# Kernel tuning notes

Measured on AMD Instinct MI355X. Metric: run time of the kernel, lower is better.

The kernel has to match this reference:

```python
import jax, jax.numpy as jnp
import numpy as np

B, S, D = 2, 4096, 1152
H = 16
HD = D // H  # 72
SCALE = HD ** -0.5


def setup_inputs() -> dict:
    key = jax.random.key(0)
    ks = jax.random.split(key, 9)
    std = 1.0 / np.sqrt(D)
    return {
        "x": jax.random.normal(ks[0], (B, S, D), dtype=jnp.float32),
        "q_w": jax.random.normal(ks[1], (D, D), dtype=jnp.float32) * std,
        "q_b": jax.random.normal(ks[2], (D,), dtype=jnp.float32) * std,
        "k_w": jax.random.normal(ks[3], (D, D), dtype=jnp.float32) * std,
        "k_b": jax.random.normal(ks[4], (D,), dtype=jnp.float32) * std,
        "v_w": jax.random.normal(ks[5], (D, D), dtype=jnp.float32) * std,
        "v_b": jax.random.normal(ks[6], (D,), dtype=jnp.float32) * std,
        "o_w": jax.random.normal(ks[7], (D, D), dtype=jnp.float32) * std,
        "o_b": jax.random.normal(ks[8], (D,), dtype=jnp.float32) * std,
    }


def reference(x, q_w, q_b, k_w, k_b, v_w, v_b, o_w, o_b):
    # Linear layers: torch nn.Linear stores weight as [out, in]; y = x @ W^T + b
    q = jnp.einsum("bsd,ed->bse", x, q_w) + q_b
    k = jnp.einsum("bsd,ed->bse", x, k_w) + k_b
    v = jnp.einsum("bsd,ed->bse", x, v_w) + v_b
    # [B, H, S, HD]
    q = q.reshape(B, S, H, HD).transpose(0, 2, 1, 3)
    k = k.reshape(B, S, H, HD).transpose(0, 2, 1, 3)
    v = v.reshape(B, S, H, HD).transpose(0, 2, 1, 3)
    # scores [B, H, S, S]
    scores = jnp.einsum("bhqd,bhkd->bhqk", q, k) * SCALE
    attn = jax.nn.softmax(scores.astype(jnp.float32), axis=-1).astype(q.dtype)
    out = jnp.einsum("bhqk,bhkd->bhqd", attn, v)
    out = out.transpose(0, 2, 1, 3).reshape(B, S, D)
    return jnp.einsum("bsd,ed->bse", out, o_w) + o_b
```

## Files before the change

### kernel.cpp

```cpp
#include <hip/hip_runtime.h>

#define NB 2
#define NS 4096
#define ND 1152
#define NH 16
#define HD 72
#define HP 80
#define VP 96
#define QSCALE (0.11785113019775793f * 1.4426950408889634f)

typedef float f32x4 __attribute__((ext_vector_type(4)));
typedef float f32x16 __attribute__((ext_vector_type(16)));
typedef __bf16 bf16x8 __attribute__((ext_vector_type(8)));
typedef unsigned short u16x8 __attribute__((ext_vector_type(8)));
typedef unsigned short u16x4 __attribute__((ext_vector_type(4)));
typedef unsigned int u32x4 __attribute__((ext_vector_type(4)));

__device__ __forceinline__ unsigned short f2bf(float f) {
  return __builtin_bit_cast(unsigned short, (__bf16)f);
}
__device__ __forceinline__ bf16x8 asbf(u16x8 u) {
  return __builtin_bit_cast(bf16x8, u);
}
__device__ __forceinline__ unsigned cvtpk(float lo, float hi) {
  unsigned d;
  asm("v_cvt_pk_bf16_f32 %0, %1, %2" : "=v"(d) : "v"(lo), "v"(hi));
  return d;
}
__device__ __forceinline__ void lane32swap(unsigned &x, unsigned &y) {
  asm volatile("v_permlane32_swap_b32 %0, %1" : "+v"(x), "+v"(y));
}
#if __has_builtin(__builtin_amdgcn_exp2f)
#define EXP2(x) __builtin_amdgcn_exp2f(x)
#else
#define EXP2(x) exp2f(x)
#endif
__device__ __forceinline__ void gll16(const void* g, void* l) {
  __builtin_amdgcn_global_load_lds(
      (__attribute__((address_space(1))) void*)(unsigned long long)g,
      (__attribute__((address_space(3))) void*)l, 16, 0, 0);
}

__global__ __launch_bounds__(256) void cvt_all(
    const float* __restrict__ x,
    const float* __restrict__ qw, const float* __restrict__ kw,
    const float* __restrict__ vw,
    unsigned short* __restrict__ xb, unsigned short* __restrict__ wb) {
  const size_t NX = (size_t)8192 * ND;
  const size_t NW = (size_t)ND * ND;
  size_t i = ((size_t)blockIdx.x * 256 + threadIdx.x) * 8;
  const float* s; unsigned short* d; size_t off;
  if (i < NX)            { s = x;  d = xb;          off = i; }
  else if (i < NX + NW)  { s = qw; d = wb;          off = i - NX; }
  else if (i < NX + 2*NW){ s = kw; d = wb + NW;     off = i - NX - NW; }
  else                   { s = vw; d = wb + 2 * NW; off = i - NX - 2 * NW; }
  f32x4 a = *(const f32x4*)(s + off);
  f32x4 b = *(const f32x4*)(s + off + 4);
  u16x8 o;
#pragma unroll
  for (int j = 0; j < 4; ++j) { o[j] = f2bf(a[j]); o[j + 4] = f2bf(b[j]); }
  *(u16x8*)(d + off) = o;
}

__global__ __launch_bounds__(256) void pad_zero(unsigned short* __restrict__ q80,
                                                unsigned short* __restrict__ k80,
                                                unsigned short* __restrict__ vt) {
  int i = blockIdx.x * 256 + threadIdx.x;
  u16x8 z = {};
  if (i < 131072) {
    *(u16x8*)(q80 + (size_t)i * HP + HD) = z;
  } else if (i < 262144) {
    *(u16x8*)(k80 + (size_t)(i - 131072) * HP + HD) = z;
  } else {
    int j = i - 262144;
    int bh = j / 12288;
    int r = j % 12288;
    int row = 72 + r / 512;
    int col = (r % 512) * 8;
    u16x8 v = z;
    if (row == HD) {
#pragma unroll
      for (int j8 = 0; j8 < 8; ++j8) v[j8] = 0x3F80;
    }
    *(u16x8*)(vt + ((size_t)bh * VP + row) * NS + col) = v;
  }
}

__global__ __launch_bounds__(256) void qk_gemm(
    const unsigned short* __restrict__ xb, const unsigned short* __restrict__ wb,
    const float* __restrict__ qbias, const float* __restrict__ kbias,
    unsigned short* __restrict__ qp, unsigned short* __restrict__ kp)
{
  const int mb = blockIdx.x * 128;
  const int nb = blockIdx.y * 128;
  const int proj = blockIdx.z;
  const unsigned short* w = wb + (size_t)proj * (ND * ND);
  const float* bias = proj == 0 ? qbias : kbias;

  __shared__ __align__(16) unsigned short la[128 * 64];
  __shared__ __align__(16) unsigned short lb[128 * 64];

  const int t = threadIdx.x;
  const int lane = t & 63;
  const int wid = t >> 6;
  const int mo = (wid >> 1) * 64, no = (wid & 1) * 64;
  const int l15 = lane & 15, l4 = lane >> 4;

  const unsigned short* ga = xb + (size_t)(mb + wid * 32 + (lane >> 3)) * ND + (lane & 7) * 8;
  const unsigned short* gb = w  + (size_t)(nb + wid * 32 + (lane >> 3)) * ND + (lane & 7) * 8;

  f32x4 acc[4][4] = {};

  for (int kt = 0; kt < ND / 64; ++kt) {
    const int k0 = kt * 64;
    __syncthreads();
#pragma unroll
    for (int j = 0; j < 4; ++j) {
      gll16(ga + (size_t)j * 8 * ND + k0, &la[(wid * 4 + j) * 512]);
      gll16(gb + (size_t)j * 8 * ND + k0, &lb[(wid * 4 + j) * 512]);
    }
    __syncthreads();
#pragma unroll
    for (int ks = 0; ks < 2; ++ks) {
      bf16x8 af[4], bfr[4];
#pragma unroll
      for (int mt = 0; mt < 4; ++mt)
        af[mt] = asbf(*(const u16x8*)(&la[(mo + mt * 16 + l15) * 64 + ks * 32 + l4 * 8]));
#pragma unroll
      for (int nt = 0; nt < 4; ++nt)
        bfr[nt] = asbf(*(const u16x8*)(&lb[(no + nt * 16 + l15) * 64 + ks * 32 + l4 * 8]));
#pragma unroll
      for (int mt = 0; mt < 4; ++mt)
#pragma unroll
        for (int nt = 0; nt < 4; ++nt)
          acc[mt][nt] = __builtin_amdgcn_mfma_f32_16x16x32_bf16(af[mt], bfr[nt], acc[mt][nt], 0, 0, 0);
    }
  }

#pragma unroll
  for (int mt = 0; mt < 4; ++mt) {
#pragma unroll
    for (int nt = 0; nt < 4; ++nt) {
      const int n = nb + no + nt * 16 + l15;
      const float bval = bias[n];
      const int h = n / HD, hd = n % HD;
#pragma unroll
      for (int r = 0; r < 4; ++r) {
        const int m = mb + mo + mt * 16 + l4 * 4 + r;
        const int b = m >> 12, sl = m & (NS - 1);
        const int bh = b * NH + h;
        float v = acc[mt][nt][r] + bval;
        if (proj == 0)
          qp[((size_t)bh * NS + sl) * HP + hd] = f2bf(v * QSCALE);
        else
          kp[((size_t)bh * NS + sl) * HP + hd] = f2bf(v);
      }
    }
  }
}

__global__ __launch_bounds__(256) void v_gemm(
    const unsigned short* __restrict__ xb, const unsigned short* __restrict__ wv,
    const float* __restrict__ vb, unsigned short* __restrict__ vt)
{
  const int mb = blockIdx.x * 128;
  const int nb = blockIdx.y * 128;

  __shared__ __align__(16) unsigned short la[128 * 64];
  __shared__ __align__(16) unsigned short lb[128 * 64];

  const int t = threadIdx.x;
  const int lane = t & 63;
  const int wid = t >> 6;
  const int mo = (wid >> 1) * 64, no = (wid & 1) * 64;
  const int l15 = lane & 15, l4 = lane >> 4;

  const unsigned short* ga = xb + (size_t)(mb + wid * 32 + (lane >> 3)) * ND + (lane & 7) * 8;
  const unsigned short* gb = wv + (size_t)(nb + wid * 32 + (lane >> 3)) * ND + (lane & 7) * 8;

  f32x4 acc[4][4] = {};

  for (int kt = 0; kt < ND / 64; ++kt) {
    const int k0 = kt * 64;
    __syncthreads();
#pragma unroll
    for (int j = 0; j < 4; ++j) {
      gll16(ga + (size_t)j * 8 * ND + k0, &la[(wid * 4 + j) * 512]);
      gll16(gb + (size_t)j * 8 * ND + k0, &lb[(wid * 4 + j) * 512]);
    }
    __syncthreads();
#pragma unroll
    for (int ks = 0; ks < 2; ++ks) {
      bf16x8 af[4], bfr[4];
#pragma unroll
      for (int mt = 0; mt < 4; ++mt)
        af[mt] = asbf(*(const u16x8*)(&la[(mo + mt * 16 + l15) * 64 + ks * 32 + l4 * 8]));
#pragma unroll
      for (int nt = 0; nt < 4; ++nt)
        bfr[nt] = asbf(*(const u16x8*)(&lb[(no + nt * 16 + l15) * 64 + ks * 32 + l4 * 8]));
#pragma unroll
      for (int mt = 0; mt < 4; ++mt)
#pragma unroll
        for (int nt = 0; nt < 4; ++nt)
          acc[mt][nt] = __builtin_amdgcn_mfma_f32_16x16x32_bf16(bfr[nt], af[mt], acc[mt][nt], 0, 0, 0);
    }
  }

#pragma unroll
  for (int mt = 0; mt < 4; ++mt) {
    const int m = mb + mo + mt * 16 + l15;
    const int b = m >> 12, sl = m & (NS - 1);
#pragma unroll
    for (int nt = 0; nt < 4; ++nt) {
#pragma unroll
      for (int r = 0; r < 4; ++r) {
        const int n = nb + no + nt * 16 + l4 * 4 + r;
        const int h = n / HD, hd = n % HD;
        vt[(((size_t)(b * NH + h)) * VP + hd) * NS + sl] =
            f2bf(acc[mt][nt][r] + vb[n]);
      }
    }
  }
}

__device__ __forceinline__ void softmax_pv(f32x16 s, const unsigned short* cur,
                                           int mt, int lane, f32x16 o[3]) {
#pragma unroll
  for (int i = 0; i < 16; ++i) s[i] = EXP2(s[i]);
  unsigned dk[8];
#pragma unroll
  for (int r2 = 0; r2 < 4; ++r2) {
    dk[2 * r2]     = cvtpk(s[4 * r2],     s[4 * r2 + 1]);
    dk[2 * r2 + 1] = cvtpk(s[4 * r2 + 2], s[4 * r2 + 3]);
  }
#pragma unroll
  for (int a = 0; a < 2; ++a) {
    unsigned x0 = dk[4 * a + 0], y0 = dk[4 * a + 2];
    unsigned x1 = dk[4 * a + 1], y1 = dk[4 * a + 3];
    lane32swap(x0, y0);
    lane32swap(x1, y1);
    u32x4 wd = {x0, x1, y0, y1};
    bf16x8 pf = __builtin_bit_cast(bf16x8, wd);
    const int ks2 = mt * 2 + a;
    __builtin_amdgcn_s_setprio(1);
#pragma unroll
    for (int hdt = 0; hdt < 3; ++hdt) {
      bf16x8 vf = asbf(*(const u16x8*)(&cur[(640 + (hdt * 4 + ks2) * 64 + lane) * 8]));
      o[hdt] = __builtin_amdgcn_mfma_f32_32x32x16_bf16(vf, pf, o[hdt], 0, 0, 0);
    }
    __builtin_amdgcn_s_setprio(0);
  }
}

__global__ __launch_bounds__(512, 4) void attn_fwd(
    const unsigned short* __restrict__ qp,
    const unsigned short* __restrict__ kp,
    const unsigned short* __restrict__ vt,
    unsigned short* __restrict__ ao)
{
  const int d = blockIdx.x;
  const int qt = (d >> 3) & 15;
  const int bh = (d & 7) + 8 * (d >> 7);
  const int b = bh >> 4, h = bh & 15;
  const int qs0 = qt * 256;

  __shared__ __align__(16) unsigned short sm[2 * 1408 * 8];

  const int t = threadIdx.x;
  const int wv = t >> 6;
  const int lane = t & 63;
  const int q = lane & 31;
  const int hh = lane >> 5;

  bf16x8 qf[5];
  {
    const unsigned short* qrow =
        qp + ((size_t)bh * NS + qs0 + wv * 32 + q) * HP + hh * 8;
#pragma unroll
    for (int ks = 0; ks < 5; ++ks)
      qf[ks] = asbf(*(const u16x8*)(qrow + ks * 16));
  }

  const unsigned short* kb0 = kp + (size_t)bh * NS * HP;
  const unsigned short* vb0 = vt + (size_t)bh * VP * NS;
  const unsigned short* gp[3];
  int stp[3], goff[3];
  const bool has2 = wv < 6;
#pragma unroll
  for (int j = 0; j < 3; ++j) {
    int g = wv + 8 * j;
    if (g > 21) g = 21;
    if (g < 10) {
      gp[j] = kb0 + ((g / 5) * 32 + (lane & 31)) * HP + (g % 5) * 16 + (lane >> 5) * 8;
      stp[j] = 64 * HP;
    } else {
      const int f = g - 10;
      gp[j] = vb0 + (size_t)((f >> 2) * 32 + (lane & 31)) * NS + (f & 3) * 16 + (lane >> 5) * 8;
      stp[j] = 64;
    }
    goff[j] = g * 512;
  }

  f32x16 o[3] = {};

  gll16(gp[0], sm + goff[0]); gp[0] += stp[0];
  gll16(gp[1], sm + goff[1]); gp[1] += stp[1];
  if (has2) { gll16(gp[2], sm + goff[2]); gp[2] += stp[2]; }
  __syncthreads();

  for (int it = 0; it < NS / 64; ++it) {
    unsigned short* cur = sm + (it & 1) * 11264;
    unsigned short* nxt = sm + ((it + 1) & 1) * 11264;
    if (it < NS / 64 - 1) {
      gll16(gp[0], nxt + goff[0]); gp[0] += stp[0];
      gll16(gp[1], nxt + goff[1]); gp[1] += stp[1];
      if (has2) { gll16(gp[2], nxt + goff[2]); gp[2] += stp[2]; }
    }

#pragma unroll
    for (int mt = 0; mt < 2; ++mt) {
      f32x16 s = {};
      __builtin_amdgcn_s_setprio(1);
#pragma unroll
      for (int ks = 0; ks < 5; ++ks) {
        bf16x8 kf = asbf(*(const u16x8*)(&cur[((mt * 5 + ks) * 64 + lane) * 8]));
        s = __builtin_amdgcn_mfma_f32_32x32x16_bf16(kf, qf[ks], s, 0, 0, 0);
      }
      __builtin_amdgcn_s_setprio(0);
      softmax_pv(s, cur, mt, lane, o);
    }
    __syncthreads();
  }

  const float l_tot = __shfl(o[2][4], q);
  const float inv = 1.0f / l_tot;
  const int srow = qs0 + wv * 32 + q;
  unsigned short* ob = ao + ((size_t)b * NS + srow) * ND + h * HD;
#pragma unroll
  for (int hdt = 0; hdt < 3; ++hdt)
#pragma unroll
    for (int r2 = 0; r2 < 4; ++r2) {
      const int hd0 = hdt * 32 + r2 * 8 + hh * 4;
      if (hd0 < HD) {
        u16x4 ov;
#pragma unroll
        for (int r0 = 0; r0 < 4; ++r0) ov[r0] = f2bf(o[hdt][r2 * 4 + r0] * inv);
        *(u16x4*)(ob + hd0) = ov;
      }
    }
}

__global__ __launch_bounds__(256) void oproj_gemm(
    const unsigned short* __restrict__ a,
    const float* __restrict__ w, const float* __restrict__ bias,
    float* __restrict__ out)
{
  const int mb = blockIdx.x * 128;
  const int nb = blockIdx.y * 128;

  __shared__ __align__(16) unsigned short la[128 * 72];
  __shared__ __align__(16) unsigned short lb[128 * 72];

  const int t = threadIdx.x;
  const int lane = t & 63;
  const int wid = t >> 6;
  const int mo = (wid >> 1) * 64, no = (wid & 1) * 64;
  const int l15 = lane & 15, l4 = lane >> 4;

  f32x4 acc[4][4] = {};

  for (int kt = 0; kt < ND / 64; ++kt) {
    const int k0 = kt * 64;
    __syncthreads();
#pragma unroll
    for (int i = 0; i < 4; ++i) {
      int c = t + i * 256;
      int row = c >> 3, c8 = c & 7;
      u16x8 ua = *(const u16x8*)(a + (size_t)(mb + row) * ND + k0 + c8 * 8);
      *(u16x8*)(&la[row * 72 + c8 * 8]) = ua;
    }
#pragma unroll
    for (int i = 0; i < 8; ++i) {
      int c = t + i * 256;
      int row = c >> 4, c4 = c & 15;
      f32x4 b4 = *(const f32x4*)(w + (size_t)(nb + row) * ND + k0 + c4 * 4);
      u16x4 ub;
#pragma unroll
      for (int j = 0; j < 4; ++j) ub[j] = f2bf(b4[j]);
      *(u16x4*)(&lb[row * 72 + c4 * 4]) = ub;
    }
    __syncthreads();
#pragma unroll
    for (int ks = 0; ks < 2; ++ks) {
      bf16x8 af[4], bfr[4];
#pragma unroll
      for (int mt = 0; mt < 4; ++mt)
        af[mt] = asbf(*(const u16x8*)(&la[(mo + mt * 16 + l15) * 72 + ks * 32 + l4 * 8]));
#pragma unroll
      for (int nt = 0; nt < 4; ++nt)
        bfr[nt] = asbf(*(const u16x8*)(&lb[(no + nt * 16 + l15) * 72 + ks * 32 + l4 * 8]));
#pragma unroll
      for (int mt = 0; mt < 4; ++mt)
#pragma unroll
        for (int nt = 0; nt < 4; ++nt)
          acc[mt][nt] = __builtin_amdgcn_mfma_f32_16x16x32_bf16(af[mt], bfr[nt], acc[mt][nt], 0, 0, 0);
    }
  }

#pragma unroll
  for (int mt = 0; mt < 4; ++mt)
#pragma unroll
    for (int nt = 0; nt < 4; ++nt) {
      const int n = nb + no + nt * 16 + l15;
      const float bval = bias[n];
#pragma unroll
      for (int r = 0; r < 4; ++r) {
        const int m = mb + mo + mt * 16 + l4 * 4 + r;
        out[(size_t)m * ND + n] = acc[mt][nt][r] + bval;
      }
    }
}

extern "C" void kernel_launch(void* const* d_in, const int* in_sizes, int n_in,
                              void* d_out, int out_size, void* d_ws, size_t ws_size,
                              hipStream_t stream) {
  const float* x  = (const float*)d_in[0];
  const float* qw = (const float*)d_in[1];
  const float* qb = (const float*)d_in[2];
  const float* kw = (const float*)d_in[3];
  const float* kb = (const float*)d_in[4];
  const float* vw = (const float*)d_in[5];
  const float* vb = (const float*)d_in[6];
  const float* ow = (const float*)d_in[7];
  const float* ob = (const float*)d_in[8];
  float* out = (float*)d_out;

  char* ws = (char*)d_ws;
  unsigned short* q80    = (unsigned short*)(ws);
  unsigned short* k80    = (unsigned short*)(ws + 20971520);
  unsigned short* v_t    = (unsigned short*)(ws + 41943040);
  unsigned short* xb     = (unsigned short*)(ws + 67108864);
  unsigned short* wb     = (unsigned short*)(ws + 85983232);

  cvt_all<<<dim3(6552), dim3(256), 0, stream>>>(x, qw, kw, vw, xb, wb);
  pad_zero<<<dim3(2560), dim3(256), 0, stream>>>(q80, k80, v_t);
  qk_gemm<<<dim3(64, 9, 2), dim3(256), 0, stream>>>(xb, wb, qb, kb, q80, k80);
  v_gemm<<<dim3(64, 9), dim3(256), 0, stream>>>(xb, wb + 2 * (size_t)ND * ND,
                                                vb, v_t);
  attn_fwd<<<dim3(512), dim3(512), 0, stream>>>(q80, k80, v_t, xb );
  oproj_gemm<<<dim3(64, 9), dim3(256), 0, stream>>>(xb , ow, ob, out);
}
```

Before: 350.4 us.

## Merge cvt/pad kernels, convert o_w in attention tail blocks, use LDS DMA in oproj

Fuses the conversion and padding kernels into one launch to save a launch. Adds 16 extra blocks to the attention grid that convert the fp32 output-projection weight to bf16 into the now-free wb buffer, overlapping with attention. The output projection then loads bf16 A and B tiles straight into LDS with global_load_lds and an unpadded 64-wide layout, dropping per-iteration fp32 conversion. The unpadded LDS layout may add bank conflicts, and the extra blocks take CUs from attention.

```diff
diff --git a/kernel.cpp b/kernel.cpp
--- a/kernel.cpp
+++ b/kernel.cpp
@@ -41,48 +41,48 @@
       (__attribute__((address_space(3))) void*)l, 16, 0, 0);
 }
 
-__global__ __launch_bounds__(256) void cvt_all(
+__global__ __launch_bounds__(256) void cvt_pad(
     const float* __restrict__ x,
     const float* __restrict__ qw, const float* __restrict__ kw,
     const float* __restrict__ vw,
-    unsigned short* __restrict__ xb, unsigned short* __restrict__ wb) {
-  const size_t NX = (size_t)8192 * ND;
-  const size_t NW = (size_t)ND * ND;
-  size_t i = ((size_t)blockIdx.x * 256 + threadIdx.x) * 8;
-  const float* s; unsigned short* d; size_t off;
-  if (i < NX)            { s = x;  d = xb;          off = i; }
-  else if (i < NX + NW)  { s = qw; d = wb;          off = i - NX; }
-  else if (i < NX + 2*NW){ s = kw; d = wb + NW;     off = i - NX - NW; }
-  else                   { s = vw; d = wb + 2 * NW; off = i - NX - 2 * NW; }
-  f32x4 a = *(const f32x4*)(s + off);
-  f32x4 b = *(const f32x4*)(s + off + 4);
-  u16x8 o;
-#pragma unroll
-  for (int j = 0; j < 4; ++j) { o[j] = f2bf(a[j]); o[j + 4] = f2bf(b[j]); }
-  *(u16x8*)(d + off) = o;
-}
-
-__global__ __launch_bounds__(256) void pad_zero(unsigned short* __restrict__ q80,
-                                                unsigned short* __restrict__ k80,
-                                                unsigned short* __restrict__ vt) {
-  int i = blockIdx.x * 256 + threadIdx.x;
-  u16x8 z = {};
-  if (i < 131072) {
-    *(u16x8*)(q80 + (size_t)i * HP + HD) = z;
-  } else if (i < 262144) {
-    *(u16x8*)(k80 + (size_t)(i - 131072) * HP + HD) = z;
+    unsigned short* __restrict__ xb, unsigned short* __restrict__ wb,
+    unsigned short* __restrict__ q80, unsigned short* __restrict__ k80,
+    unsigned short* __restrict__ vt) {
+  if (blockIdx.x < 6552) {
+    const size_t NX = (size_t)8192 * ND;
+    const size_t NW = (size_t)ND * ND;
+    size_t i = ((size_t)blockIdx.x * 256 + threadIdx.x) * 8;
+    const float* s; unsigned short* d; size_t off;
+    if (i < NX)            { s = x;  d = xb;          off = i; }
+    else if (i < NX + NW)  { s = qw; d = wb;          off = i - NX; }
+    else if (i < NX + 2*NW){ s = kw; d = wb + NW;     off = i - NX - NW; }
+    else                   { s = vw; d = wb + 2 * NW; off = i - NX - 2 * NW; }
+    f32x4 a = *(const f32x4*)(s + off);
+    f32x4 b = *(const f32x4*)(s + off + 4);
+    u16x8 o;
+#pragma unroll
+    for (int j = 0; j < 4; ++j) { o[j] = f2bf(a[j]); o[j + 4] = f2bf(b[j]); }
+    *(u16x8*)(d + off) = o;
   } else {
-    int j = i - 262144;
-    int bh = j / 12288;
-    int r = j % 12288;
-    int row = 72 + r / 512;
-    int col = (r % 512) * 8;
-    u16x8 v = z;
-    if (row == HD) {
-#pragma unroll
-      for (int j8 = 0; j8 < 8; ++j8) v[j8] = 0x3F80;
-    }
-    *(u16x8*)(vt + ((size_t)bh * VP + row) * NS + col) = v;
+    int i = (blockIdx.x - 6552) * 256 + threadIdx.x;
+    u16x8 z = {};
+    if (i < 131072) {
+      *(u16x8*)(q80 + (size_t)i * HP + HD) = z;
+    } else if (i < 262144) {
+      *(u16x8*)(k80 + (size_t)(i - 131072) * HP + HD) = z;
+    } else {
+      int j = i - 262144;
+      int bh = j / 12288;
+      int r = j % 12288;
+      int row = 72 + r / 512;
+      int col = (r % 512) * 8;
+      u16x8 v = z;
+      if (row == HD) {
+#pragma unroll
+        for (int j8 = 0; j8 < 8; ++j8) v[j8] = 0x3F80;
+      }
+      *(u16x8*)(vt + ((size_t)bh * VP + row) * NS + col) = v;
+    }
   }
 }
 
@@ -256,8 +256,23 @@
     const unsigned short* __restrict__ qp,
     const unsigned short* __restrict__ kp,
     const unsigned short* __restrict__ vt,
-    unsigned short* __restrict__ ao)
+    unsigned short* __restrict__ ao,
+    const float* __restrict__ ow, unsigned short* __restrict__ owb)
 {
+  if (blockIdx.x >= 512) {
+    const int tid = (blockIdx.x - 512) * 512 + threadIdx.x;
+    for (size_t c = tid; c < (size_t)ND * ND / 8; c += 8192) {
+      size_t off = c * 8;
+      f32x4 a = *(const f32x4*)(ow + off);
+      f32x4 b = *(const f32x4*)(ow + off + 4);
+      u16x8 o;
+#pragma unroll
+      for (int j = 0; j < 4; ++j) { o[j] = f2bf(a[j]); o[j + 4] = f2bf(b[j]); }
+      *(u16x8*)(owb + off) = o;
+    }
+    return;
+  }
+
   const int d = blockIdx.x;
   const int qt = (d >> 3) & 15;
   const int bh = (d & 7) + 8 * (d >> 7);
@@ -352,14 +367,14 @@
 
 __global__ __launch_bounds__(256) void oproj_gemm(
     const unsigned short* __restrict__ a,
-    const float* __restrict__ w, const float* __restrict__ bias,
+    const unsigned short* __restrict__ wbf, const float* __restrict__ bias,
     float* __restrict__ out)
 {
   const int mb = blockIdx.x * 128;
   const int nb = blockIdx.y * 128;
 
-  __shared__ __align__(16) unsigned short la[128 * 72];
-  __shared__ __align__(16) unsigned short lb[128 * 72];
+  __shared__ __align__(16) unsigned short la[128 * 64];
+  __shared__ __align__(16) unsigned short lb[128 * 64];
 
   const int t = threadIdx.x;
   const int lane = t & 63;
@@ -367,27 +382,18 @@
   const int mo = (wid >> 1) * 64, no = (wid & 1) * 64;
   const int l15 = lane & 15, l4 = lane >> 4;
 
+  const unsigned short* ga = a   + (size_t)(mb + wid * 32 + (lane >> 3)) * ND + (lane & 7) * 8;
+  const unsigned short* gb = wbf + (size_t)(nb + wid * 32 + (lane >> 3)) * ND + (lane & 7) * 8;
+
   f32x4 acc[4][4] = {};
 
   for (int kt = 0; kt < ND / 64; ++kt) {
     const int k0 = kt * 64;
     __syncthreads();
 #pragma unroll
-    for (int i = 0; i < 4; ++i) {
-      int c = t + i * 256;
-      int row = c >> 3, c8 = c & 7;
-      u16x8 ua = *(const u16x8*)(a + (size_t)(mb + row) * ND + k0 + c8 * 8);
-      *(u16x8*)(&la[row * 72 + c8 * 8]) = ua;
-    }
-#pragma unroll
-    for (int i = 0; i < 8; ++i) {
-      int c = t + i * 256;
-      int row = c >> 4, c4 = c & 15;
-      f32x4 b4 = *(const f32x4*)(w + (size_t)(nb + row) * ND + k0 + c4 * 4);
-      u16x4 ub;
-#pragma unroll
-      for (int j = 0; j < 4; ++j) ub[j] = f2bf(b4[j]);
-      *(u16x4*)(&lb[row * 72 + c4 * 4]) = ub;
+    for (int j = 0; j < 4; ++j) {
+      gll16(ga + (size_t)j * 8 * ND + k0, &la[(wid * 4 + j) * 512]);
+      gll16(gb + (size_t)j * 8 * ND + k0, &lb[(wid * 4 + j) * 512]);
     }
     __syncthreads();
 #pragma unroll
@@ -395,10 +401,10 @@
       bf16x8 af[4], bfr[4];
 #pragma unroll
       for (int mt = 0; mt < 4; ++mt)
-        af[mt] = asbf(*(const u16x8*)(&la[(mo + mt * 16 + l15) * 72 + ks * 32 + l4 * 8]));
+        af[mt] = asbf(*(const u16x8*)(&la[(mo + mt * 16 + l15) * 64 + ks * 32 + l4 * 8]));
 #pragma unroll
       for (int nt = 0; nt < 4; ++nt)
-        bfr[nt] = asbf(*(const u16x8*)(&lb[(no + nt * 16 + l15) * 72 + ks * 32 + l4 * 8]));
+        bfr[nt] = asbf(*(const u16x8*)(&lb[(no + nt * 16 + l15) * 64 + ks * 32 + l4 * 8]));
 #pragma unroll
       for (int mt = 0; mt < 4; ++mt)
 #pragma unroll
@@ -442,11 +448,12 @@
   unsigned short* xb     = (unsigned short*)(ws + 67108864);
   unsigned short* wb     = (unsigned short*)(ws + 85983232);
 
-  cvt_all<<<dim3(6552), dim3(256), 0, stream>>>(x, qw, kw, vw, xb, wb);
-  pad_zero<<<dim3(2560), dim3(256), 0, stream>>>(q80, k80, v_t);
+  cvt_pad<<<dim3(9112), dim3(256), 0, stream>>>(x, qw, kw, vw, xb, wb,
+                                                q80, k80, v_t);
   qk_gemm<<<dim3(64, 9, 2), dim3(256), 0, stream>>>(xb, wb, qb, kb, q80, k80);
   v_gemm<<<dim3(64, 9), dim3(256), 0, stream>>>(xb, wb + 2 * (size_t)ND * ND,
                                                 vb, v_t);
-  attn_fwd<<<dim3(512), dim3(512), 0, stream>>>(q80, k80, v_t, xb );
-  oproj_gemm<<<dim3(64, 9), dim3(256), 0, stream>>>(xb , ow, ob, out);
-}
+  attn_fwd<<<dim3(528), dim3(512), 0, stream>>>(q80, k80, v_t, xb ,
+                                                ow, wb );
+  oproj_gemm<<<dim3(64, 9), dim3(256), 0, stream>>>(xb , wb, ob, out);
+}
```

New measurement: 334.4 us. 4.6% less time.
